# Kernel tuning notes

Hardware: AMD Instinct MI355X
Metric: run time of the kernel (lower is better)

Reference implementation:

```python
import jax, jax.numpy as jnp
import numpy as np
from jax import lax

DIM = 1024
D_STATE = 64
D_CONV = 4
EXPAND = 2
HEADDIM = 64
D_INNER = EXPAND * DIM            # 2048
NHEADS = D_INNER // HEADDIM       # 32
NGROUPS = 1
CONV_DIM = D_INNER + 2 * NGROUPS * D_STATE      # 2176
D_IN_PROJ = 2 * D_INNER + 2 * NGROUPS * D_STATE + NHEADS  # 4256
BATCH, SEQLEN = 2, 4096
EPS = 1e-5


def setup_inputs() -> dict:
    key = jax.random.key(0)
    ks = jax.random.split(key, 10)
    X = jax.random.normal(ks[0], (BATCH, SEQLEN, DIM), dtype=jnp.float32)
    in_proj_w = jax.random.normal(ks[1], (D_IN_PROJ, DIM), dtype=jnp.float32) * 0.02
    conv_w = jax.random.normal(ks[2], (CONV_DIM, 1, D_CONV), dtype=jnp.float32) * 0.2
    conv_b = jax.random.normal(ks[3], (CONV_DIM,), dtype=jnp.float32) * 0.02
    dt_bias = jax.random.normal(ks[4], (NHEADS,), dtype=jnp.float32) * 0.5 - 2.0
    A_log = jnp.log(jax.random.uniform(ks[5], (NHEADS,), minval=1.0, maxval=16.0))
    D = jax.random.normal(ks[6], (NHEADS,), dtype=jnp.float32)
    norm_w = jnp.ones((D_INNER,), dtype=jnp.float32)
    out_proj_w = jax.random.normal(ks[7], (DIM, D_INNER), dtype=jnp.float32) * 0.02
    to_h_w = jax.random.normal(ks[8], (2 * DIM, DIM), dtype=jnp.float32) * 0.02
    return dict(X=X, in_proj_w=in_proj_w, conv_w=conv_w, conv_b=conv_b,
                dt_bias=dt_bias, A_log=A_log, D=D, norm_w=norm_w,
                out_proj_w=out_proj_w, to_h_w=to_h_w)


def _silu(x):
    return x * jax.nn.sigmoid(x)


def _mamba2(X, in_proj_w, conv_w, conv_b, dt_bias, A_log, D, norm_w, out_proj_w):
    Bsz, L, _ = X.shape
    zxbcdt = jnp.einsum('bld,ed->ble', X, in_proj_w)  # (B,L,D_IN_PROJ)
    z = zxbcdt[..., :D_INNER]
    xBC = zxbcdt[..., D_INNER:D_INNER + CONV_DIM]
    dt_raw = zxbcdt[..., D_INNER + CONV_DIM:]
    dt = jax.nn.softplus(dt_raw + dt_bias)  # (B,L,H)

    # causal depthwise conv over time, then silu
    xc = jnp.transpose(xBC, (0, 2, 1))                       # (B,C,L)
    xc = jnp.pad(xc, ((0, 0), (0, 0), (D_CONV - 1, 0)))
    xc = lax.conv_general_dilated(xc, conv_w, window_strides=(1,), padding='VALID',
                                  dimension_numbers=('NCH', 'OIH', 'NCH'),
                                  feature_group_count=CONV_DIM)
    xc = xc + conv_b[None, :, None]
    xBC = _silu(jnp.transpose(xc, (0, 2, 1)))                # (B,L,C)

    x = xBC[..., :D_INNER].reshape(Bsz, L, NHEADS, HEADDIM)  # (B,L,H,P)
    Bm = xBC[..., D_INNER:D_INNER + D_STATE]                 # (B,L,N) ngroups=1
    Cm = xBC[..., D_INNER + D_STATE:]                        # (B,L,N)

    A = -jnp.exp(A_log)                                      # (H,)

    def step(h, inp):
        dt_t, B_t, C_t, x_t = inp   # (B,H), (B,N), (B,N), (B,H,P)
        dA = jnp.exp(dt_t * A)                               # (B,H)
        h = h * dA[..., None, None] + jnp.einsum('bh,bhp,bn->bhpn', dt_t, x_t, B_t)
        y_t = jnp.einsum('bhpn,bn->bhp', h, C_t)
        return h, y_t

    h0 = jnp.zeros((Bsz, NHEADS, HEADDIM, D_STATE), dtype=X.dtype)
    xs = (jnp.moveaxis(dt, 1, 0), jnp.moveaxis(Bm, 1, 0),
          jnp.moveaxis(Cm, 1, 0), jnp.moveaxis(x, 1, 0))
    _, ys = lax.scan(step, h0, xs)                           # (L,B,H,P)
    y = jnp.moveaxis(ys, 0, 1) + x * D[None, None, :, None]  # skip term
    y = y.reshape(Bsz, L, D_INNER)

    # gated RMSNorm: rmsnorm(y * silu(z)) * weight
    y = y * _silu(z)
    y = y * lax.rsqrt(jnp.mean(y * y, axis=-1, keepdims=True) + EPS) * norm_w
    return jnp.einsum('bld,ed->ble', y, out_proj_w)          # (B,L,DIM)


def reference(X, in_proj_w, conv_w, conv_b, dt_bias, A_log, D, norm_w, out_proj_w, to_h_w):
    H = _mamba2(X, in_proj_w, conv_w, conv_b, dt_bias, A_log, D, norm_w, out_proj_w)
    HKV = jnp.einsum('bld,ed->ble', H, to_h_w)               # (B,L,2*DIM)
    HK, HV = HKV[..., :DIM], HKV[..., DIM:]
    return (HK, HV)
```

## Files before the change

### kernel.cpp

```cpp
#include <hip/hip_runtime.h>
#include <hip/hip_bf16.h>
#include <math.h>

#define B_       2
#define L_       4096
#define DIM_     1024
#define DINNER_  2048
#define DSTATE_  64
#define NH_      32
#define HD_      64
#define CONVDIM_ 2176
#define DIP_     4256
#define M_       (B_*L_)
#define XRW_     2208
#define NC_      64

typedef __attribute__((ext_vector_type(8))) short short8;
typedef __attribute__((ext_vector_type(4))) float floatx4;
typedef __hip_bfloat16 bf16;

__device__ __forceinline__ float bf2f(unsigned short u) {
    unsigned int v = ((unsigned int)u) << 16;
    return __builtin_bit_cast(float, v);
}
__device__ __forceinline__ unsigned short f2bf(float f) {
    unsigned int x = __builtin_bit_cast(unsigned int, f);
    unsigned int lsb = (x >> 16) & 1u;
    x += 0x7fffu + lsb;
    return (unsigned short)(x >> 16);
}
__device__ __forceinline__ void storeo(bf16* p, float v) {
    *reinterpret_cast<unsigned short*>(p) = f2bf(v);
}
__device__ __forceinline__ void storeo(float* p, float v) { *p = v; }

__device__ __forceinline__ void gl2lds16(const bf16* g, short* lds) {
    __builtin_amdgcn_global_load_lds(
        (const __attribute__((address_space(1))) void*)g,
        (__attribute__((address_space(3))) void*)lds, 16, 0, 0);
}

__global__ __launch_bounds__(256) void cast_f32_bf16_k(
    const float* __restrict__ src, bf16* __restrict__ dst)
{
    size_t i0 = ((size_t)blockIdx.x * 256 + threadIdx.x) * 8;
    uint4 a = *reinterpret_cast<const uint4*>(src + i0);
    uint4 b = *reinterpret_cast<const uint4*>(src + i0 + 4);
    unsigned int w0 = (unsigned int)f2bf(__builtin_bit_cast(float, a.x)) |
                      ((unsigned int)f2bf(__builtin_bit_cast(float, a.y)) << 16);
    unsigned int w1 = (unsigned int)f2bf(__builtin_bit_cast(float, a.z)) |
                      ((unsigned int)f2bf(__builtin_bit_cast(float, a.w)) << 16);
    unsigned int w2 = (unsigned int)f2bf(__builtin_bit_cast(float, b.x)) |
                      ((unsigned int)f2bf(__builtin_bit_cast(float, b.y)) << 16);
    unsigned int w3 = (unsigned int)f2bf(__builtin_bit_cast(float, b.z)) |
                      ((unsigned int)f2bf(__builtin_bit_cast(float, b.w)) << 16);
    *reinterpret_cast<uint4*>(reinterpret_cast<unsigned short*>(dst) + i0) =
        make_uint4(w0, w1, w2, w3);
}

template <typename TO>
__global__ __launch_bounds__(256) void gemm_bt16(
    const bf16* __restrict__ A, const bf16* __restrict__ W,
    TO* __restrict__ outA, TO* __restrict__ outB,
    int M, int N, int K, int split, int strideA, int strideB)
{
    __shared__ short As[128*64];
    __shared__ short Ws[128*64];
    const int tid  = threadIdx.x;
    const int m0   = blockIdx.y * 128;
    const int n0   = blockIdx.x * 128;
    const int wave = tid >> 6;
    const int lane = tid & 63;
    const int wm   = (wave >> 1) * 64;
    const int wn   = (wave & 1) * 64;
    const int ln   = lane & 15;
    const int quad = lane >> 4;
    const int lr   = lane >> 3;
    const int lc   = (lane & 7) * 8;

    floatx4 acc[4][4];
#pragma unroll
    for (int i = 0; i < 4; i++)
#pragma unroll
        for (int j = 0; j < 4; j++) acc[i][j] = (floatx4){0.f, 0.f, 0.f, 0.f};

    for (int k0 = 0; k0 < K; k0 += 64) {
#pragma unroll
        for (int it = 0; it < 4; it++) {
            int ig = wave * 4 + it;
            gl2lds16(A + (size_t)(m0 + ig * 8 + lr) * K + k0 + lc, &As[ig * 512]);
            gl2lds16(W + (size_t)(n0 + ig * 8 + lr) * K + k0 + lc, &Ws[ig * 512]);
        }
        __syncthreads();
#pragma unroll
        for (int kk = 0; kk < 64; kk += 32) {
            short8 af[4], bfv[4];
#pragma unroll
            for (int i = 0; i < 4; i++)
                af[i] = *reinterpret_cast<const short8*>(&As[(wm + i * 16 + ln) * 64 + kk + quad * 8]);
#pragma unroll
            for (int j = 0; j < 4; j++)
                bfv[j] = *reinterpret_cast<const short8*>(&Ws[(wn + j * 16 + ln) * 64 + kk + quad * 8]);
#pragma unroll
            for (int i = 0; i < 4; i++)
#pragma unroll
                for (int j = 0; j < 4; j++)
                    acc[i][j] = __builtin_amdgcn_mfma_f32_16x16x32_bf16(af[i], bfv[j], acc[i][j], 0, 0, 0);
        }
        __syncthreads();
    }

#pragma unroll
    for (int i = 0; i < 4; i++)
#pragma unroll
        for (int j = 0; j < 4; j++)
#pragma unroll
            for (int r = 0; r < 4; r++) {
                int grow = m0 + wm + i * 16 + quad * 4 + r;
                int gcol = n0 + wn + j * 16 + ln;
                if (gcol < N) {
                    if (gcol < split)
                        storeo(outA + (size_t)grow * strideA + gcol, acc[i][j][r]);
                    else
                        storeo(outB + (size_t)grow * strideB + (gcol - split), acc[i][j][r]);
                }
            }
}

__global__ __launch_bounds__(256) void chunk_intra_k(
    const bf16* __restrict__ xr,
    const float* __restrict__ cw, const float* __restrict__ cb,
    const float* __restrict__ dtb, const float* __restrict__ A_log,
    const float* __restrict__ Dp,
    bf16* __restrict__ Yg, float* __restrict__ Sg, bf16* __restrict__ Cg,
    float* __restrict__ wcumG, float* __restrict__ Eg)
{
    __shared__ short Bst[64*72];
    __shared__ short Cst[64*72];
    __shared__ short xT [64*72];
    __shared__ short BwT[64*72];
    __shared__ unsigned short raw[3*67*64];
    __shared__ float wXc[256], wBc[256], wCc[256];
    __shared__ float bXc[64], bBc[64], bCc[64];
    __shared__ float dts[64], cums[64], wS[64], wcumS[64];

    const int tid  = threadIdx.x;
    const int bid  = blockIdx.x;
    const int h    = bid & 31;
    const int bc   = bid >> 5;
    const int c    = bc & 63;
    const int b    = bc >> 6;
    const int xch0 = h * 64;
    const unsigned short* xru = (const unsigned short*)xr;

    const float Ah   = -__expf(A_log[h]);
    const float Dh   = Dp[h];
    const float dtbh = dtb[h];

    { int n = tid >> 2, j = tid & 3;
      wXc[tid] = cw[(xch0 + n) * 4 + j];
      wBc[tid] = cw[(2048 + n) * 4 + j];
      wCc[tid] = cw[(2112 + n) * 4 + j]; }
    if (tid < 64) { bXc[tid] = cb[xch0 + tid]; bBc[tid] = cb[2048 + tid]; bCc[tid] = cb[2112 + tid]; }

    for (int q = tid; q < 536; q += 256) {
        int r = q >> 3, c8 = (q & 7) * 8;
        int rt = c * 64 - 3 + r;
        uint4 vX = make_uint4(0u,0u,0u,0u), vB = vX, vC = vX;
        if (rt >= 0) {
            size_t ro = (size_t)(b * L_ + rt) * XRW_;
            vX = *reinterpret_cast<const uint4*>(xru + ro + xch0 + c8);
            vB = *reinterpret_cast<const uint4*>(xru + ro + 2048 + c8);
            vC = *reinterpret_cast<const uint4*>(xru + ro + 2112 + c8);
        }
        *reinterpret_cast<uint4*>(&raw[r*64 + c8])        = vX;
        *reinterpret_cast<uint4*>(&raw[4288 + r*64 + c8]) = vB;
        *reinterpret_cast<uint4*>(&raw[8576 + r*64 + c8]) = vC;
    }
    if (tid < 64) {
        float v = bf2f(xru[(size_t)(b * L_ + c * 64 + tid) * XRW_ + 2176 + h]) + dtbh;
        dts[tid] = fmaxf(v, 0.f) + log1pf(__expf(-fabsf(v)));
    }
    __syncthreads();

    if (tid == 0) {
        float cc = 0.f;
        for (int t = 0; t < 64; t++) { cc += dts[t] * Ah; cums[t] = cc; }
    }
    __syncthreads();
    if (tid < 64) {
        wS[tid]    = __expf(cums[63] - cums[tid]) * dts[tid];
        wcumS[tid] = __expf(cums[tid]);
        wcumG[(size_t)bid * 64 + tid] = wcumS[tid];
    }
    if (tid == 0) Eg[bid] = __expf(cums[63]);
    __syncthreads();

    for (int q = tid; q < 12288; q += 256) {
        int mtx = q >> 12;
        int qq  = q & 4095;
        int s = qq >> 6, ch = qq & 63;
        if (mtx == 0) {
            float a = bBc[ch];
#pragma unroll
            for (int j = 0; j < 4; j++) a = fmaf(bf2f(raw[4288 + (s+j)*64 + ch]), wBc[ch*4+j], a);
            float sv = a / (1.f + __expf(-a));
            Bst[s*72 + ch] = f2bf(sv);
            BwT[ch*72 + s] = f2bf(sv * wS[s]);
        } else if (mtx == 1) {
            float a = bCc[ch];
#pragma unroll
            for (int j = 0; j < 4; j++) a = fmaf(bf2f(raw[8576 + (s+j)*64 + ch]), wCc[ch*4+j], a);
            float sv = a / (1.f + __expf(-a));
            unsigned short u = f2bf(sv);
            Cst[s*72 + ch] = u;
            if (h == 0) ((unsigned short*)Cg)[(size_t)(b*L_ + c*64 + s)*64 + ch] = u;
        } else {
            float a = bXc[ch];
#pragma unroll
            for (int j = 0; j < 4; j++) a = fmaf(bf2f(raw[(s+j)*64 + ch]), wXc[ch*4+j], a);
            float sv = a / (1.f + __expf(-a));
            xT[ch*72 + s] = f2bf(sv);
        }
    }
    __syncthreads();

    const int wave = tid >> 6, lane = tid & 63;
    const int ln = lane & 15, quad = lane >> 4;
    const int wm = (wave >> 1) * 32, wn = (wave & 1) * 32;

    floatx4 accG[2][2];
#pragma unroll
    for (int i = 0; i < 2; i++)
#pragma unroll
        for (int j = 0; j < 2; j++) accG[i][j] = (floatx4){0.f,0.f,0.f,0.f};
#pragma unroll
    for (int kk = 0; kk < 64; kk += 32) {
        short8 af[2], bfv[2];
#pragma unroll
        for (int i = 0; i < 2; i++)
            af[i] = *reinterpret_cast<const short8*>(&Cst[(wm + i*16 + ln)*72 + kk + quad*8]);
#pragma unroll
        for (int j = 0; j < 2; j++)
            bfv[j] = *reinterpret_cast<const short8*>(&Bst[(wn + j*16 + ln)*72 + kk + quad*8]);
#pragma unroll
        for (int i = 0; i < 2; i++)
#pragma unroll
            for (int j = 0; j < 2; j++)
                accG[i][j] = __builtin_amdgcn_mfma_f32_16x16x32_bf16(af[i], bfv[j], accG[i][j], 0,0,0);
    }
    short* Mm = (short*)raw;
#pragma unroll
    for (int i = 0; i < 2; i++)
#pragma unroll
        for (int j = 0; j < 2; j++)
#pragma unroll
            for (int r = 0; r < 4; r++) {
                int t = wm + i*16 + quad*4 + r;
                int s = wn + j*16 + ln;
                float v = (s <= t) ? __expf(cums[t] - cums[s]) * dts[s] * accG[i][j][r] : 0.f;
                Mm[t*72 + s] = (short)f2bf(v);
            }
    __syncthreads();

    floatx4 accY[2][2];
#pragma unroll
    for (int i = 0; i < 2; i++)
#pragma unroll
        for (int j = 0; j < 2; j++) accY[i][j] = (floatx4){0.f,0.f,0.f,0.f};
#pragma unroll
    for (int kk = 0; kk < 64; kk += 32) {
        short8 af[2], bfv[2];
#pragma unroll
        for (int i = 0; i < 2; i++)
            af[i] = *reinterpret_cast<const short8*>(&Mm[(wm + i*16 + ln)*72 + kk + quad*8]);
#pragma unroll
        for (int j = 0; j < 2; j++)
            bfv[j] = *reinterpret_cast<const short8*>(&xT[(wn + j*16 + ln)*72 + kk + quad*8]);
#pragma unroll
        for (int i = 0; i < 2; i++)
#pragma unroll
            for (int j = 0; j < 2; j++)
                accY[i][j] = __builtin_amdgcn_mfma_f32_16x16x32_bf16(af[i], bfv[j], accY[i][j], 0,0,0);
    }
    unsigned short* Yu = (unsigned short*)Yg;
#pragma unroll
    for (int i = 0; i < 2; i++)
#pragma unroll
        for (int j = 0; j < 2; j++)
#pragma unroll
            for (int r = 0; r < 4; r++) {
                int t = wm + i*16 + quad*4 + r;
                int p = wn + j*16 + ln;
                float yv = accY[i][j][r] + Dh * bf2f((unsigned short)xT[p*72 + t]);
                Yu[(size_t)(b*L_ + c*64 + t)*DINNER_ + xch0 + p] = f2bf(yv);
            }

    floatx4 accS[2][2];
#pragma unroll
    for (int i = 0; i < 2; i++)
#pragma unroll
        for (int j = 0; j < 2; j++) accS[i][j] = (floatx4){0.f,0.f,0.f,0.f};
#pragma unroll
    for (int kk = 0; kk < 64; kk += 32) {
        short8 af[2], bfv[2];
#pragma unroll
        for (int i = 0; i < 2; i++)
            af[i] = *reinterpret_cast<const short8*>(&xT[(wm + i*16 + ln)*72 + kk + quad*8]);
#pragma unroll
        for (int j = 0; j < 2; j++)
            bfv[j] = *reinterpret_cast<const short8*>(&BwT[(wn + j*16 + ln)*72 + kk + quad*8]);
#pragma unroll
        for (int i = 0; i < 2; i++)
#pragma unroll
            for (int j = 0; j < 2; j++)
                accS[i][j] = __builtin_amdgcn_mfma_f32_16x16x32_bf16(af[i], bfv[j], accS[i][j], 0,0,0);
    }
#pragma unroll
    for (int i = 0; i < 2; i++)
#pragma unroll
        for (int j = 0; j < 2; j++)
#pragma unroll
            for (int r = 0; r < 4; r++) {
                int p = wm + i*16 + quad*4 + r;
                int n = wn + j*16 + ln;
                Sg[(size_t)bid * 4096 + p*64 + n] = accS[i][j][r];
            }
}

__global__ __launch_bounds__(256) void chunk_state_k(
    float* __restrict__ Sg, const float* __restrict__ Eg)
{
    int g  = blockIdx.x * 1024 + threadIdx.x * 4;
    int bh = g >> 12;
    int b  = bh >> 5, h = bh & 31;
    int e  = g & 4095;
    float4 run = make_float4(0.f, 0.f, 0.f, 0.f);
    for (int c = 0; c < NC_; c++) {
        int bid = (b * 64 + c) * 32 + h;
        size_t idx = (size_t)bid * 4096 + e;
        float4 s = *reinterpret_cast<float4*>(&Sg[idx]);
        float  E = Eg[bid];
        *reinterpret_cast<float4*>(&Sg[idx]) = run;
        run.x = run.x * E + s.x;
        run.y = run.y * E + s.y;
        run.z = run.z * E + s.z;
        run.w = run.w * E + s.w;
    }
}

__global__ __launch_bounds__(256) void chunk_inter_k(
    const bf16* __restrict__ Cg, const float* __restrict__ Sg,
    const float* __restrict__ wcumG, bf16* __restrict__ Yg)
{
    __shared__ short Cst[64*72];
    __shared__ short hpT[64*72];
    __shared__ float wcumL[64];

    const int tid = threadIdx.x;
    const int bid = blockIdx.x;
    const int h   = bid & 31;
    const int bc  = bid >> 5;
    const int c   = bc & 63;
    const int b   = bc >> 6;

    for (int q = tid; q < 512; q += 256) {
        int r = q >> 3, c8 = (q & 7) * 8;
        *reinterpret_cast<uint4*>(&Cst[r*72 + c8]) =
            *reinterpret_cast<const uint4*>((const unsigned short*)Cg + (size_t)(b*L_ + c*64 + r)*64 + c8);
    }
    for (int q = tid; q < 1024; q += 256) {
        int p = q >> 4, n4 = (q & 15) * 4;
        float4 v = *reinterpret_cast<const float4*>(&Sg[(size_t)bid * 4096 + p*64 + n4]);
        unsigned int lo = (unsigned int)f2bf(v.x) | ((unsigned int)f2bf(v.y) << 16);
        unsigned int hi = (unsigned int)f2bf(v.z) | ((unsigned int)f2bf(v.w) << 16);
        *reinterpret_cast<uint2*>(&hpT[p*72 + n4]) = make_uint2(lo, hi);
    }
    if (tid < 64) wcumL[tid] = wcumG[(size_t)bid * 64 + tid];
    __syncthreads();

    const int wave = tid >> 6, lane = tid & 63;
    const int ln = lane & 15, quad = lane >> 4;
    const int wm = (wave >> 1) * 32, wn = (wave & 1) * 32;

    floatx4 acc[2][2];
#pragma unroll
    for (int i = 0; i < 2; i++)
#pragma unroll
        for (int j = 0; j < 2; j++) acc[i][j] = (floatx4){0.f,0.f,0.f,0.f};
#pragma unroll
    for (int kk = 0; kk < 64; kk += 32) {
        short8 af[2], bfv[2];
#pragma unroll
        for (int i = 0; i < 2; i++)
            af[i] = *reinterpret_cast<const short8*>(&Cst[(wm + i*16 + ln)*72 + kk + quad*8]);
#pragma unroll
        for (int j = 0; j < 2; j++)
            bfv[j] = *reinterpret_cast<const short8*>(&hpT[(wn + j*16 + ln)*72 + kk + quad*8]);
#pragma unroll
        for (int i = 0; i < 2; i++)
#pragma unroll
            for (int j = 0; j < 2; j++)
                acc[i][j] = __builtin_amdgcn_mfma_f32_16x16x32_bf16(af[i], bfv[j], acc[i][j], 0,0,0);
    }
    unsigned short* Yu = (unsigned short*)Yg;
#pragma unroll
    for (int i = 0; i < 2; i++)
#pragma unroll
        for (int j = 0; j < 2; j++)
#pragma unroll
            for (int r = 0; r < 4; r++) {
                int t = wm + i*16 + quad*4 + r;
                int p = wn + j*16 + ln;
                size_t idx = (size_t)(b*L_ + c*64 + t)*DINNER_ + h*64 + p;
                float yv = bf2f(Yu[idx]) + wcumL[t] * acc[i][j][r];
                Yu[idx] = f2bf(yv);
            }
}

__global__ __launch_bounds__(256) void gate_norm_k(
    bf16* __restrict__ y, const bf16* __restrict__ zbuf, const float* __restrict__ nw)
{
    __shared__ float red[4];
    int row = blockIdx.x;
    int tid = threadIdx.x;
    unsigned short* yy = (unsigned short*)y;
    const unsigned short* zz = (const unsigned short*)zbuf;

    uint4 yv = *reinterpret_cast<uint4*>(&yy[(size_t)row * DINNER_ + tid * 8]);
    uint4 zv = *reinterpret_cast<const uint4*>(&zz[(size_t)row * DINNER_ + tid * 8]);
    unsigned int yw[4] = {yv.x, yv.y, yv.z, yv.w};
    unsigned int zw[4] = {zv.x, zv.y, zv.z, zv.w};
    float g[8];
    float ss = 0.f;
#pragma unroll
    for (int q = 0; q < 4; q++) {
        float y0 = bf2f((unsigned short)(yw[q] & 0xffffu)), y1 = bf2f((unsigned short)(yw[q] >> 16));
        float z0 = bf2f((unsigned short)(zw[q] & 0xffffu)), z1 = bf2f((unsigned short)(zw[q] >> 16));
        float g0 = y0 * (z0 / (1.f + __expf(-z0)));
        float g1 = y1 * (z1 / (1.f + __expf(-z1)));
        g[q * 2] = g0; g[q * 2 + 1] = g1;
        ss += g0 * g0 + g1 * g1;
    }
#pragma unroll
    for (int o = 1; o < 64; o <<= 1) ss += __shfl_xor(ss, o);
    if ((tid & 63) == 0) red[tid >> 6] = ss;
    __syncthreads();
    float tot = red[0] + red[1] + red[2] + red[3];
    float rinv = rsqrtf(tot * (1.f / DINNER_) + 1e-5f);

    unsigned int ow[4];
#pragma unroll
    for (int q = 0; q < 4; q++) {
        float w0 = nw[tid * 8 + q * 2];
        float w1 = nw[tid * 8 + q * 2 + 1];
        unsigned short o0 = f2bf(g[q * 2] * rinv * w0);
        unsigned short o1 = f2bf(g[q * 2 + 1] * rinv * w1);
        ow[q] = (unsigned int)o0 | ((unsigned int)o1 << 16);
    }
    *reinterpret_cast<uint4*>(&yy[(size_t)row * DINNER_ + tid * 8]) =
        make_uint4(ow[0], ow[1], ow[2], ow[3]);
}


extern "C" void kernel_launch(void* const* d_in, const int* in_sizes, int n_in,
                              void* d_out, int out_size, void* d_ws, size_t ws_size,
                              hipStream_t stream)
{
    const float* X    = (const float*)d_in[0];
    const float* Wip  = (const float*)d_in[1];
    const float* cw   = (const float*)d_in[2];
    const float* cb   = (const float*)d_in[3];
    const float* dtb  = (const float*)d_in[4];
    const float* Alog = (const float*)d_in[5];
    const float* Dp   = (const float*)d_in[6];
    const float* nw   = (const float*)d_in[7];
    const float* Wop  = (const float*)d_in[8];
    const float* Wth  = (const float*)d_in[9];
    float* out = (float*)d_out;

    char* ws = (char*)d_ws;
    bf16*  zbuf  = (bf16*) (ws);
    bf16*  Wopb  = (bf16*) (ws);
    bf16*  Wthb  = (bf16*) (ws + 4194304);
    bf16*  xr    = (bf16*) (ws + 33554432);
    bf16*  Hbuf  = (bf16*) (ws + 33554432);
    bf16*  Yg    = (bf16*) (ws + 69730304);
    bf16*  Xb    = (bf16*) (ws + 69730304);
    bf16*  Wipb  = (bf16*) (ws + 69730304 + 16777216);
    bf16*  Cg    = (bf16*) (ws + 103284736);
    float* wcumG = (float*)(ws + 104333312);
    float* Eg    = (float*)(ws + 106430464);
    float* Sg    = (float*)d_out;

    dim3 blk(256);

    cast_f32_bf16_k<<<(M_ * DIM_) / 2048, blk, 0, stream>>>(X, Xb);
    cast_f32_bf16_k<<<(DIP_ * DIM_) / 2048, blk, 0, stream>>>(Wip, Wipb);

    gemm_bt16<bf16><<<dim3(34, M_ / 128), blk, 0, stream>>>(
        Xb, Wipb, zbuf, xr, M_, DIP_, DIM_, DINNER_, DINNER_, XRW_);

    chunk_intra_k<<<B_ * NC_ * NH_, blk, 0, stream>>>(
        xr, cw, cb, dtb, Alog, Dp, Yg, Sg, Cg, wcumG, Eg);
    chunk_state_k<<<256, blk, 0, stream>>>(Sg, Eg);
    chunk_inter_k<<<B_ * NC_ * NH_, blk, 0, stream>>>(Cg, Sg, wcumG, Yg);

    gate_norm_k<<<M_, blk, 0, stream>>>(Yg, zbuf, nw);

    cast_f32_bf16_k<<<(DIM_ * DINNER_) / 2048, blk, 0, stream>>>(Wop, Wopb);
    cast_f32_bf16_k<<<(DINNER_ * DIM_) / 2048, blk, 0, stream>>>(Wth, Wthb);

    gemm_bt16<bf16><<<dim3(DIM_ / 128, M_ / 128), blk, 0, stream>>>(
        Yg, Wopb, Hbuf, Hbuf, M_, DIM_, DINNER_, DIM_, DIM_, DIM_);

    gemm_bt16<float><<<dim3(DINNER_ / 128, M_ / 128), blk, 0, stream>>>(
        Hbuf, Wthb, out, out + (size_t)M_ * DIM_, M_, DINNER_, DIM_, DIM_, DIM_, DIM_);
}
```

Before: 544.0 us.

## Hoist causal conv and softplus dt into standalone kernels before chunk scan

Adds a conv_all_k kernel that computes the depthwise causal conv plus SiLU once for all channels, and a dt_k kernel that computes softplus(dt) once. Previously every (batch, chunk, head) block recomputed the B and C conv, which is 32x redundant across heads. chunk_intra_k now only loads precomputed tiles and transposes them. chunk_inter_k recomputes the cumulative decay locally instead of reading a stored wcum buffer. The cost is two extra launches and an extra round trip of the conv output through global memory, plus a repeated serial cumsum in the inter kernel.

```diff
diff --git a/kernel.cpp b/kernel.cpp
--- a/kernel.cpp
+++ b/kernel.cpp
@@ -127,22 +127,66 @@
             }
 }
 
+__global__ __launch_bounds__(256) void conv_all_k(
+    const bf16* __restrict__ xr, const float* __restrict__ cw,
+    const float* __restrict__ cb, bf16* __restrict__ xc)
+{
+    int idx = blockIdx.x * 256 + threadIdx.x;
+    int row = idx / 272;
+    int ch0 = (idx - row * 272) * 8;
+    int t   = row & (L_ - 1);
+    const unsigned short* xru = (const unsigned short*)xr;
+    uint4 rv[4];
+#pragma unroll
+    for (int j = 0; j < 4; j++) {
+        rv[j] = make_uint4(0u, 0u, 0u, 0u);
+        if (t + j - 3 >= 0)
+            rv[j] = *reinterpret_cast<const uint4*>(xru + (size_t)(row + j - 3) * XRW_ + ch0);
+    }
+    unsigned int ow[4];
+#pragma unroll
+    for (int pair = 0; pair < 4; pair++) {
+        unsigned short o2[2];
+#pragma unroll
+        for (int k = 0; k < 2; k++) {
+            int cc = pair * 2 + k;
+            float a = cb[ch0 + cc];
+#pragma unroll
+            for (int j = 0; j < 4; j++) {
+                unsigned int w32 = (&rv[j].x)[cc >> 1];
+                unsigned short u = (cc & 1) ? (unsigned short)(w32 >> 16)
+                                            : (unsigned short)(w32 & 0xffffu);
+                a = fmaf(bf2f(u), cw[(ch0 + cc) * 4 + j], a);
+            }
+            o2[k] = f2bf(a / (1.f + __expf(-a)));
+        }
+        ow[pair] = (unsigned int)o2[0] | ((unsigned int)o2[1] << 16);
+    }
+    *reinterpret_cast<uint4*>((unsigned short*)xc + (size_t)row * CONVDIM_ + ch0) =
+        make_uint4(ow[0], ow[1], ow[2], ow[3]);
+}
+
+__global__ __launch_bounds__(256) void dt_k(
+    const bf16* __restrict__ xr, const float* __restrict__ dtb, float* __restrict__ dtf)
+{
+    int idx = blockIdx.x * 256 + threadIdx.x;
+    int h  = idx & (NH_ - 1);
+    int ml = idx >> 5;
+    float v = bf2f(((const unsigned short*)xr)[(size_t)ml * XRW_ + 2176 + h]) + dtb[h];
+    dtf[idx] = fmaxf(v, 0.f) + log1pf(__expf(-fabsf(v)));
+}
+
 __global__ __launch_bounds__(256) void chunk_intra_k(
-    const bf16* __restrict__ xr,
-    const float* __restrict__ cw, const float* __restrict__ cb,
-    const float* __restrict__ dtb, const float* __restrict__ A_log,
-    const float* __restrict__ Dp,
-    bf16* __restrict__ Yg, float* __restrict__ Sg, bf16* __restrict__ Cg,
-    float* __restrict__ wcumG, float* __restrict__ Eg)
+    const bf16* __restrict__ xc, const float* __restrict__ dtf,
+    const float* __restrict__ A_log, const float* __restrict__ Dp,
+    bf16* __restrict__ Yg, float* __restrict__ Sg, float* __restrict__ Eg)
 {
     __shared__ short Bst[64*72];
     __shared__ short Cst[64*72];
+    __shared__ short xsM[64*72];
     __shared__ short xT [64*72];
     __shared__ short BwT[64*72];
-    __shared__ unsigned short raw[3*67*64];
-    __shared__ float wXc[256], wBc[256], wCc[256];
-    __shared__ float bXc[64], bBc[64], bCc[64];
-    __shared__ float dts[64], cums[64], wS[64], wcumS[64];
+    __shared__ float dts[64], cums[64], wS[64];
 
     const int tid  = threadIdx.x;
     const int bid  = blockIdx.x;
@@ -151,36 +195,27 @@
     const int c    = bc & 63;
     const int b    = bc >> 6;
     const int xch0 = h * 64;
-    const unsigned short* xru = (const unsigned short*)xr;
-
-    const float Ah   = -__expf(A_log[h]);
-    const float Dh   = Dp[h];
-    const float dtbh = dtb[h];
-
-    { int n = tid >> 2, j = tid & 3;
-      wXc[tid] = cw[(xch0 + n) * 4 + j];
-      wBc[tid] = cw[(2048 + n) * 4 + j];
-      wCc[tid] = cw[(2112 + n) * 4 + j]; }
-    if (tid < 64) { bXc[tid] = cb[xch0 + tid]; bBc[tid] = cb[2048 + tid]; bCc[tid] = cb[2112 + tid]; }
-
-    for (int q = tid; q < 536; q += 256) {
-        int r = q >> 3, c8 = (q & 7) * 8;
-        int rt = c * 64 - 3 + r;
-        uint4 vX = make_uint4(0u,0u,0u,0u), vB = vX, vC = vX;
-        if (rt >= 0) {
-            size_t ro = (size_t)(b * L_ + rt) * XRW_;
-            vX = *reinterpret_cast<const uint4*>(xru + ro + xch0 + c8);
-            vB = *reinterpret_cast<const uint4*>(xru + ro + 2048 + c8);
-            vC = *reinterpret_cast<const uint4*>(xru + ro + 2112 + c8);
-        }
-        *reinterpret_cast<uint4*>(&raw[r*64 + c8])        = vX;
-        *reinterpret_cast<uint4*>(&raw[4288 + r*64 + c8]) = vB;
-        *reinterpret_cast<uint4*>(&raw[8576 + r*64 + c8]) = vC;
-    }
-    if (tid < 64) {
-        float v = bf2f(xru[(size_t)(b * L_ + c * 64 + tid) * XRW_ + 2176 + h]) + dtbh;
-        dts[tid] = fmaxf(v, 0.f) + log1pf(__expf(-fabsf(v)));
-    }
+    const unsigned short* xcu = (const unsigned short*)xc;
+
+    const float Ah = -__expf(A_log[h]);
+    const float Dh = Dp[h];
+
+    for (int q = tid; q < 1536; q += 256) {
+        int sel = q >> 9;
+        int qq  = q & 511;
+        int r = qq >> 3, c8 = (qq & 7) * 8;
+        size_t ro = (size_t)(b * L_ + c * 64 + r) * CONVDIM_;
+        if (sel == 0)
+            *reinterpret_cast<uint4*>(&Bst[r*72 + c8]) =
+                *reinterpret_cast<const uint4*>(xcu + ro + 2048 + c8);
+        else if (sel == 1)
+            *reinterpret_cast<uint4*>(&Cst[r*72 + c8]) =
+                *reinterpret_cast<const uint4*>(xcu + ro + 2112 + c8);
+        else
+            *reinterpret_cast<uint4*>(&xsM[r*72 + c8]) =
+                *reinterpret_cast<const uint4*>(xcu + ro + xch0 + c8);
+    }
+    if (tid < 64) dts[tid] = dtf[(size_t)(b * L_ + c * 64 + tid) * NH_ + h];
     __syncthreads();
 
     if (tid == 0) {
@@ -188,40 +223,14 @@
         for (int t = 0; t < 64; t++) { cc += dts[t] * Ah; cums[t] = cc; }
     }
     __syncthreads();
-    if (tid < 64) {
-        wS[tid]    = __expf(cums[63] - cums[tid]) * dts[tid];
-        wcumS[tid] = __expf(cums[tid]);
-        wcumG[(size_t)bid * 64 + tid] = wcumS[tid];
-    }
+    if (tid < 64) wS[tid] = __expf(cums[63] - cums[tid]) * dts[tid];
     if (tid == 0) Eg[bid] = __expf(cums[63]);
     __syncthreads();
 
-    for (int q = tid; q < 12288; q += 256) {
-        int mtx = q >> 12;
-        int qq  = q & 4095;
-        int s = qq >> 6, ch = qq & 63;
-        if (mtx == 0) {
-            float a = bBc[ch];
-#pragma unroll
-            for (int j = 0; j < 4; j++) a = fmaf(bf2f(raw[4288 + (s+j)*64 + ch]), wBc[ch*4+j], a);
-            float sv = a / (1.f + __expf(-a));
-            Bst[s*72 + ch] = f2bf(sv);
-            BwT[ch*72 + s] = f2bf(sv * wS[s]);
-        } else if (mtx == 1) {
-            float a = bCc[ch];
-#pragma unroll
-            for (int j = 0; j < 4; j++) a = fmaf(bf2f(raw[8576 + (s+j)*64 + ch]), wCc[ch*4+j], a);
-            float sv = a / (1.f + __expf(-a));
-            unsigned short u = f2bf(sv);
-            Cst[s*72 + ch] = u;
-            if (h == 0) ((unsigned short*)Cg)[(size_t)(b*L_ + c*64 + s)*64 + ch] = u;
-        } else {
-            float a = bXc[ch];
-#pragma unroll
-            for (int j = 0; j < 4; j++) a = fmaf(bf2f(raw[(s+j)*64 + ch]), wXc[ch*4+j], a);
-            float sv = a / (1.f + __expf(-a));
-            xT[ch*72 + s] = f2bf(sv);
-        }
+    for (int q = tid; q < 4096; q += 256) {
+        int s = q & 63, ch = q >> 6;
+        xT [ch*72 + s] = xsM[s*72 + ch];
+        BwT[ch*72 + s] = (short)f2bf(bf2f((unsigned short)Bst[s*72 + ch]) * wS[s]);
     }
     __syncthreads();
 
@@ -249,7 +258,7 @@
             for (int j = 0; j < 2; j++)
                 accG[i][j] = __builtin_amdgcn_mfma_f32_16x16x32_bf16(af[i], bfv[j], accG[i][j], 0,0,0);
     }
-    short* Mm = (short*)raw;
+    __syncthreads();
 #pragma unroll
     for (int i = 0; i < 2; i++)
 #pragma unroll
@@ -259,7 +268,7 @@
                 int t = wm + i*16 + quad*4 + r;
                 int s = wn + j*16 + ln;
                 float v = (s <= t) ? __expf(cums[t] - cums[s]) * dts[s] * accG[i][j][r] : 0.f;
-                Mm[t*72 + s] = (short)f2bf(v);
+                xsM[t*72 + s] = (short)f2bf(v);
             }
     __syncthreads();
 
@@ -273,7 +282,7 @@
         short8 af[2], bfv[2];
 #pragma unroll
         for (int i = 0; i < 2; i++)
-            af[i] = *reinterpret_cast<const short8*>(&Mm[(wm + i*16 + ln)*72 + kk + quad*8]);
+            af[i] = *reinterpret_cast<const short8*>(&xsM[(wm + i*16 + ln)*72 + kk + quad*8]);
 #pragma unroll
         for (int j = 0; j < 2; j++)
             bfv[j] = *reinterpret_cast<const short8*>(&xT[(wn + j*16 + ln)*72 + kk + quad*8]);
@@ -350,12 +359,13 @@
 }
 
 __global__ __launch_bounds__(256) void chunk_inter_k(
-    const bf16* __restrict__ Cg, const float* __restrict__ Sg,
-    const float* __restrict__ wcumG, bf16* __restrict__ Yg)
+    const bf16* __restrict__ xc, const float* __restrict__ Sg,
+    const float* __restrict__ dtf, const float* __restrict__ A_log,
+    bf16* __restrict__ Yg)
 {
     __shared__ short Cst[64*72];
     __shared__ short hpT[64*72];
-    __shared__ float wcumL[64];
+    __shared__ float dts[64], cums[64], wcumL[64];
 
     const int tid = threadIdx.x;
     const int bid = blockIdx.x;
@@ -363,11 +373,14 @@
     const int bc  = bid >> 5;
     const int c   = bc & 63;
     const int b   = bc >> 6;
+    const unsigned short* xcu = (const unsigned short*)xc;
+
+    const float Ah = -__expf(A_log[h]);
 
     for (int q = tid; q < 512; q += 256) {
         int r = q >> 3, c8 = (q & 7) * 8;
         *reinterpret_cast<uint4*>(&Cst[r*72 + c8]) =
-            *reinterpret_cast<const uint4*>((const unsigned short*)Cg + (size_t)(b*L_ + c*64 + r)*64 + c8);
+            *reinterpret_cast<const uint4*>(xcu + (size_t)(b*L_ + c*64 + r)*CONVDIM_ + 2112 + c8);
     }
     for (int q = tid; q < 1024; q += 256) {
         int p = q >> 4, n4 = (q & 15) * 4;
@@ -376,7 +389,14 @@
         unsigned int hi = (unsigned int)f2bf(v.z) | ((unsigned int)f2bf(v.w) << 16);
         *reinterpret_cast<uint2*>(&hpT[p*72 + n4]) = make_uint2(lo, hi);
     }
-    if (tid < 64) wcumL[tid] = wcumG[(size_t)bid * 64 + tid];
+    if (tid < 64) dts[tid] = dtf[(size_t)(b*L_ + c*64 + tid) * NH_ + h];
+    __syncthreads();
+    if (tid == 0) {
+        float cc = 0.f;
+        for (int t = 0; t < 64; t++) { cc += dts[t] * Ah; cums[t] = cc; }
+    }
+    __syncthreads();
+    if (tid < 64) wcumL[tid] = __expf(cums[tid]);
     __syncthreads();
 
     const int wave = tid >> 6, lane = tid & 63;
@@ -480,18 +500,18 @@
     float* out = (float*)d_out;
 
     char* ws = (char*)d_ws;
-    bf16*  zbuf  = (bf16*) (ws);
-    bf16*  Wopb  = (bf16*) (ws);
-    bf16*  Wthb  = (bf16*) (ws + 4194304);
-    bf16*  xr    = (bf16*) (ws + 33554432);
-    bf16*  Hbuf  = (bf16*) (ws + 33554432);
-    bf16*  Yg    = (bf16*) (ws + 69730304);
-    bf16*  Xb    = (bf16*) (ws + 69730304);
-    bf16*  Wipb  = (bf16*) (ws + 69730304 + 16777216);
-    bf16*  Cg    = (bf16*) (ws + 103284736);
-    float* wcumG = (float*)(ws + 104333312);
-    float* Eg    = (float*)(ws + 106430464);
-    float* Sg    = (float*)d_out;
+    bf16*  zbuf = (bf16*) (ws);
+    bf16*  Wopb = (bf16*) (ws);
+    bf16*  Wthb = (bf16*) (ws + 4194304);
+    bf16*  xr   = (bf16*) (ws + 33554432);
+    bf16*  Yg   = (bf16*) (ws + 33554432);
+    bf16*  xc   = (bf16*) (ws + 69730304);
+    bf16*  Xb   = (bf16*) (ws + 69730304);
+    bf16*  Wipb = (bf16*) (ws + 69730304 + 16777216);
+    bf16*  Hbuf = (bf16*) (ws + 69730304);
+    float* dtf  = (float*)(ws + 105381888);
+    float* Eg   = (float*)(ws + 106430464);
+    float* Sg   = (float*)d_out;
 
     dim3 blk(256);
 
@@ -501,10 +521,13 @@
     gemm_bt16<bf16><<<dim3(34, M_ / 128), blk, 0, stream>>>(
         Xb, Wipb, zbuf, xr, M_, DIP_, DIM_, DINNER_, DINNER_, XRW_);
 
+    dt_k<<<(M_ * NH_) / 256, blk, 0, stream>>>(xr, dtb, dtf);
+    conv_all_k<<<(M_ * 272) / 256, blk, 0, stream>>>(xr, cw, cb, xc);
+
     chunk_intra_k<<<B_ * NC_ * NH_, blk, 0, stream>>>(
-        xr, cw, cb, dtb, Alog, Dp, Yg, Sg, Cg, wcumG, Eg);
+        xc, dtf, Alog, Dp, Yg, Sg, Eg);
     chunk_state_k<<<256, blk, 0, stream>>>(Sg, Eg);
-    chunk_inter_k<<<B_ * NC_ * NH_, blk, 0, stream>>>(Cg, Sg, wcumG, Yg);
+    chunk_inter_k<<<B_ * NC_ * NH_, blk, 0, stream>>>(xc, Sg, dtf, Alog, Yg);
 
     gate_norm_k<<<M_, blk, 0, stream>>>(Yg, zbuf, nw);
 
```

Result: faster. 513.8 us (-5.5%).
